# Performance work log

Measured on AMD Instinct MI355X. Metric: run time of the kernel, lower is better.

The kernel has to match this reference:

```python
import jax, jax.numpy as jnp
import numpy as np

B, S, T, E, H = 2, 2048, 2048, 1024, 16
D = E // H  # head_dim = 64


def setup_inputs() -> dict:
    key = jax.random.key(0)
    ks = jax.random.split(key, 11)
    scale = 1.0 / np.sqrt(E)
    return {
        "query": jax.random.normal(ks[0], (B, S, E), jnp.float32),
        "value": jax.random.normal(ks[1], (B, T, E), jnp.float32),
        "key": jax.random.normal(ks[2], (B, T, E), jnp.float32),
        "Wq": jax.random.normal(ks[3], (E, E), jnp.float32) * scale,
        "bq": jnp.zeros((E,), jnp.float32),
        "Wk": jax.random.normal(ks[4], (E, E), jnp.float32) * scale,
        "bk": jnp.zeros((E,), jnp.float32),
        "Wv": jax.random.normal(ks[5], (E, E), jnp.float32) * scale,
        "bv": jnp.zeros((E,), jnp.float32),
        "Wo": jax.random.normal(ks[6], (E, E), jnp.float32) * scale,
        "bo": jnp.zeros((E,), jnp.float32),
    }


def reference(query, value, key, Wq, bq, Wk, bk, Wv, bv, Wo, bo):
    b, s, e = query.shape
    t = value.shape[1]
    # linear projections (torch Linear: x @ W.T + b)
    q = query @ Wq.T + bq
    k = key @ Wk.T + bk
    v = value @ Wv.T + bv
    # split heads: [B, H, S, D]
    q = q.reshape(b, s, H, D).transpose(0, 2, 1, 3)
    k = k.reshape(b, t, H, D).transpose(0, 2, 1, 3)
    v = v.reshape(b, t, H, D).transpose(0, 2, 1, 3)
    # scaled dot-product attention; full [B,H,S,T] scores as in the original
    A = jnp.einsum("bhsd,bhtd->bhst", q, k) / jnp.sqrt(jnp.float32(D))
    A = jax.nn.softmax(A, axis=-1)
    # dropout p=0.0 -> identity
    out = jnp.einsum("bhst,bhtd->bhsd", A, v)
    out = out.transpose(0, 2, 1, 3).reshape(b, s, e)
    return out @ Wo.T + bo
```

## Files before the change

### kernel.cpp

```cpp
#include <hip/hip_runtime.h>
#include <math.h>

typedef __attribute__((ext_vector_type(8))) short short8;
typedef __attribute__((ext_vector_type(4))) float f32x4;
typedef unsigned short u16;

__device__ __forceinline__ u16 f2bf(float x) {
    unsigned int u = __float_as_uint(x);
    u += 0x7FFFu + ((u >> 16) & 1u);
    return (u16)(u >> 16);
}

__device__ __forceinline__ unsigned cvt_pk_bf16(float lo, float hi) {
    unsigned r;
    asm("v_cvt_pk_bf16_f32 %0, %1, %2" : "=v"(r) : "v"(lo), "v"(hi));
    return r;
}

__device__ __forceinline__ void load_lds16(const void* g, void* l) {
    __builtin_amdgcn_global_load_lds(
        (const __attribute__((address_space(1))) unsigned int*)g,
        (__attribute__((address_space(3))) unsigned int*)l,
        16, 0, 0);
}

struct CvtArgs {
    const float* src[7];
    u16* dst[7];
    int n8[7];
};

__global__ __launch_bounds__(256) void cvt_bf16(CvtArgs c) {
    const int z = blockIdx.z;
    const int i = blockIdx.x * 256 + threadIdx.x;
    if (i >= c.n8[z]) return;
    const float4* s = (const float4*)c.src[z];
    const float4 a = s[2 * i];
    const float4 b = s[2 * i + 1];
    union { short8 v; unsigned u[4]; } o;
    o.u[0] = cvt_pk_bf16(a.x, a.y);
    o.u[1] = cvt_pk_bf16(a.z, a.w);
    o.u[2] = cvt_pk_bf16(b.x, b.y);
    o.u[3] = cvt_pk_bf16(b.z, b.w);
    ((short8*)c.dst[z])[i] = o.v;
}

struct GemmArgs {
    const u16* A[3];
    const u16* W[3];
    const float* bias[3];
    void* C[3];
    float scale[3];
    int trans[3];
};

template <bool BF16OUT>
__global__ __launch_bounds__(256) void gemm_nt_mfma(GemmArgs ga, int M, int N, int K)
{
    __shared__ u16 As[128 * 32];
    __shared__ u16 Bs[128 * 32];
    const int z = blockIdx.z;
    const u16* __restrict__ A = ga.A[z];
    const u16* __restrict__ W = ga.W[z];
    const float* __restrict__ bias = ga.bias[z];
    const float scale = ga.scale[z];
    const int trans = ga.trans[z];

    const int tid = threadIdx.x;
    const int w = tid >> 6, l = tid & 63;
    const int l4 = l >> 4, lm = l & 15;
    const int wr = w >> 1, wc = w & 1;

    const int idx = blockIdx.x;
    const int xcd = idx & 7;
    const int sl  = idx >> 3;
    const int bmi = xcd * 4 + (sl & 3);
    const int bni = sl >> 2;
    const int bm = (trans ? bni : bmi) * 128;
    const int bn = (trans ? bmi : bni) * 128;

    const int srow = l >> 2;
    const int sseg = l & 3;

    f32x4 acc[4][4];
#pragma unroll
    for (int m = 0; m < 4; ++m)
#pragma unroll
        for (int n = 0; n < 4; ++n) acc[m][n] = (f32x4){0.f, 0.f, 0.f, 0.f};

    for (int k0 = 0; k0 < K; k0 += 32) {
        __syncthreads();
#pragma unroll
        for (int i = 0; i < 2; ++i) {
            const int blk = w * 2 + i;
            const int row = blk * 16 + srow;
            load_lds16(A + (size_t)(bm + row) * K + k0 + sseg * 8,
                       (char*)As + blk * 1024);
            load_lds16(W + (size_t)(bn + row) * K + k0 + sseg * 8,
                       (char*)Bs + blk * 1024);
        }
        __syncthreads();

        short8 af[4], bf[4];
#pragma unroll
        for (int m = 0; m < 4; ++m)
            af[m] = *(const short8*)&As[(wr * 64 + m * 16 + lm) * 32 + l4 * 8];
#pragma unroll
        for (int n = 0; n < 4; ++n)
            bf[n] = *(const short8*)&Bs[(wc * 64 + n * 16 + lm) * 32 + l4 * 8];
#pragma unroll
        for (int m = 0; m < 4; ++m)
#pragma unroll
            for (int n = 0; n < 4; ++n)
                acc[m][n] = __builtin_amdgcn_mfma_f32_16x16x32_bf16(af[m], bf[n], acc[m][n], 0, 0, 0);
    }

    if (!trans) {
        float bv[4];
#pragma unroll
        for (int n = 0; n < 4; ++n) bv[n] = bias[bn + wc * 64 + n * 16 + lm];
#pragma unroll
        for (int m = 0; m < 4; ++m) {
#pragma unroll
            for (int n = 0; n < 4; ++n) {
                const int col = bn + wc * 64 + n * 16 + lm;
#pragma unroll
                for (int r = 0; r < 4; ++r) {
                    const int row = bm + wr * 64 + m * 16 + l4 * 4 + r;
                    const float v = (acc[m][n][r] + bv[n]) * scale;
                    if (BF16OUT)
                        ((u16*)ga.C[z])[(size_t)row * N + col] = f2bf(v);
                    else
                        ((float*)ga.C[z])[(size_t)row * N + col] = v;
                }
            }
        }
    } else {
#pragma unroll
        for (int m = 0; m < 4; ++m) {
            const float4 bv4 = *(const float4*)(bias + bm + wr * 64 + m * 16 + l4 * 4);
            const float bvr[4] = {bv4.x, bv4.y, bv4.z, bv4.w};
#pragma unroll
            for (int n = 0; n < 4; ++n) {
                const int col = bn + wc * 64 + n * 16 + lm;
                const size_t cbase = (size_t)(col >> 11) * 2097152 + (size_t)(col & 2047);
#pragma unroll
                for (int r = 0; r < 4; ++r) {
                    const int row = bm + wr * 64 + m * 16 + l4 * 4 + r;
                    const float v = (acc[m][n][r] + bvr[r]) * scale;
                    ((u16*)ga.C[z])[cbase + (size_t)row * 2048] = f2bf(v);
                }
            }
        }
    }
}

__global__ __launch_bounds__(512, 4) void flash_attn_mfma8(
    const u16* __restrict__ Qb, const u16* __restrict__ Kb,
    const u16* __restrict__ Vt, u16* __restrict__ Ob)
{
    __shared__ u16 Ks[2][128 * 64];
    __shared__ u16 Vs[2][64 * 128];

    const int tid = threadIdx.x;
    const int w  = tid >> 6;
    const int l  = tid & 63;
    const int l4 = l >> 4;
    const int lm = l & 15;

    const int id = blockIdx.x;
    const int xcd = id & 7;
    const int s = id >> 3;
    const int qt = s & 15;
    const int g0 = (s >> 4) * 8 + xcd;
    const int h = g0 & 15;
    const int b = g0 >> 4;
    const int qb0 = qt << 7;

    const size_t bbase = (size_t)b * 2048 * 1024 + (size_t)h * 64;
    const size_t vbase = (size_t)b * 2097152 + (size_t)(h * 64) * 2048;

    short8 qf[2];
    {
        const u16* qrow = Qb + bbase + (size_t)(qb0 + w * 16 + lm) * 1024;
        qf[0] = *(const short8*)(qrow + l4 * 8);
        qf[1] = *(const short8*)(qrow + 32 + l4 * 8);
    }

    auto stageK = [&](int t0, int bufi) {
#pragma unroll
        for (int ii = 0; ii < 2; ++ii) {
            const int i = w * 2 + ii;
            const int key = i * 8 + (l >> 3);
            const int chunk = (l & 7) ^ ((l >> 3) & 7);
            load_lds16(Kb + bbase + (size_t)(t0 + key) * 1024 + chunk * 8,
                       (char*)&Ks[bufi][0] + i * 1024);
        }
    };
    auto stageV = [&](int t0, int bufi) {
#pragma unroll
        for (int ii = 0; ii < 2; ++ii) {
            const int i = w * 2 + ii;
            const int d = i * 4 + (l >> 4);
            const int chunk = (l & 15) ^ (d & 7);
            load_lds16(Vt + vbase + (size_t)d * 2048 + t0 + chunk * 8,
                       (char*)&Vs[bufi][0] + i * 1024);
        }
    };

    f32x4 oacc[4];
#pragma unroll
    for (int g = 0; g < 4; ++g) oacc[g] = (f32x4){0.f, 0.f, 0.f, 0.f};
    float m_run = -1e30f;
    float l_run = 0.f;

    stageK(0, 0);
    stageV(0, 0);

    for (int t = 0; t < 16; ++t) {
        const int buf = t & 1;
        if (t < 15) {
            stageK((t + 1) * 128, buf ^ 1);
            stageV((t + 1) * 128, buf ^ 1);
            asm volatile("s_waitcnt vmcnt(4)" ::: "memory");
        } else {
            asm volatile("s_waitcnt vmcnt(0)" ::: "memory");
        }
        __builtin_amdgcn_s_barrier();

        f32x4 sacc[8];
#pragma unroll
        for (int g = 0; g < 8; ++g) sacc[g] = (f32x4){0.f, 0.f, 0.f, 0.f};
        __builtin_amdgcn_s_setprio(1);
#pragma unroll
        for (int g = 0; g < 8; ++g) {
#pragma unroll
            for (int c = 0; c < 2; ++c) {
                const short8 kf = *(const short8*)
                    &Ks[buf][(16 * g + lm) * 64 + (((4 * c + l4) ^ (lm & 7)) << 3)];
                sacc[g] = __builtin_amdgcn_mfma_f32_16x16x32_bf16(kf, qf[c], sacc[g], 0, 0, 0);
            }
        }
        __builtin_amdgcn_s_setprio(0);

        float amax[8];
#pragma unroll
        for (int g = 0; g < 8; ++g)
            amax[g] = fmaxf(fmaxf(sacc[g][0], sacc[g][1]), fmaxf(sacc[g][2], sacc[g][3]));
        float mt = fmaxf(fmaxf(fmaxf(amax[0], amax[1]), fmaxf(amax[2], amax[3])),
                         fmaxf(fmaxf(amax[4], amax[5]), fmaxf(amax[6], amax[7])));
        mt = fmaxf(mt, __shfl_xor(mt, 16));
        mt = fmaxf(mt, __shfl_xor(mt, 32));

        const bool resc = !__all(mt <= m_run + 8.0f);
        if (resc) {
            const float mn = fmaxf(m_run, mt);
            const float alpha = __builtin_amdgcn_exp2f(m_run - mn);
            m_run = mn;
            l_run *= alpha;
#pragma unroll
            for (int r = 0; r < 4; ++r) {
                const float a = __shfl(alpha, l4 * 4 + r);
#pragma unroll
                for (int g = 0; g < 4; ++g) oacc[g][r] *= a;
            }
        }

        float lsum = 0.f;
        const float mr = m_run;
        unsigned up[8], vp[8];
#pragma unroll
        for (int g = 0; g < 8; ++g) {
            const float p0 = __builtin_amdgcn_exp2f(sacc[g][0] - mr);
            const float p1 = __builtin_amdgcn_exp2f(sacc[g][1] - mr);
            const float p2 = __builtin_amdgcn_exp2f(sacc[g][2] - mr);
            const float p3 = __builtin_amdgcn_exp2f(sacc[g][3] - mr);
            lsum += (p0 + p1) + (p2 + p3);
            up[g] = cvt_pk_bf16(p0, p1);
            vp[g] = cvt_pk_bf16(p2, p3);
        }
        lsum += __shfl_xor(lsum, 16);
        lsum += __shfl_xor(lsum, 32);
        l_run += lsum;

#pragma unroll
        for (int kb = 0; kb < 4; ++kb) {
            unsigned w0 = up[2 * kb], w2 = up[2 * kb + 1];
            unsigned w1 = vp[2 * kb], w3 = vp[2 * kb + 1];
            asm("v_permlane32_swap_b32 %0, %1" : "+v"(w0), "+v"(w2));
            asm("v_permlane16_swap_b32 %0, %1" : "+v"(w0), "+v"(w2));
            asm("v_permlane32_swap_b32 %0, %1" : "+v"(w1), "+v"(w3));
            asm("v_permlane16_swap_b32 %0, %1" : "+v"(w1), "+v"(w3));
            union { unsigned u[4]; short8 v8; } pa;
            pa.u[0] = w0; pa.u[1] = w1; pa.u[2] = w2; pa.u[3] = w3;
            __builtin_amdgcn_s_setprio(1);
#pragma unroll
            for (int g = 0; g < 4; ++g) {
                const int d = 16 * g + lm;
                const short8 vf = *(const short8*)
                    &Vs[buf][d * 128 + (((kb * 4 + l4) ^ (d & 7)) << 3)];
                oacc[g] = __builtin_amdgcn_mfma_f32_16x16x32_bf16(pa.v8, vf, oacc[g], 0, 0, 0);
            }
            __builtin_amdgcn_s_setprio(0);
        }

        __builtin_amdgcn_s_barrier();
    }

#pragma unroll
    for (int r = 0; r < 4; ++r) {
        const float linv = 1.f / __shfl(l_run, l4 * 4 + r);
        const size_t orow = bbase + (size_t)(qb0 + w * 16 + l4 * 4 + r) * 1024;
#pragma unroll
        for (int g = 0; g < 4; ++g)
            Ob[orow + g * 16 + lm] = f2bf(oacc[g][r] * linv);
    }
}

extern "C" void kernel_launch(void* const* d_in, const int* in_sizes, int n_in,
                              void* d_out, int out_size, void* d_ws, size_t ws_size,
                              hipStream_t stream)
{
    const float* query = (const float*)d_in[0];
    const float* value = (const float*)d_in[1];
    const float* key   = (const float*)d_in[2];
    const float* Wq = (const float*)d_in[3];
    const float* bq = (const float*)d_in[4];
    const float* Wk = (const float*)d_in[5];
    const float* bk = (const float*)d_in[6];
    const float* Wv = (const float*)d_in[7];
    const float* bv = (const float*)d_in[8];
    const float* Wo = (const float*)d_in[9];
    const float* bo = (const float*)d_in[10];
    float* out = (float*)d_out;

    const int M = 2 * 2048;
    const int E = 1024;
    const size_t act = (size_t)M * E;
    const size_t wel = (size_t)E * E;

    u16* qc  = (u16*)d_ws;
    u16* kc  = qc + act;
    u16* vc  = kc + act;
    u16* wqb = vc + act;
    u16* wkb = wqb + wel;
    u16* wvb = wkb + wel;
    u16* wob = wvb + wel;
    u16* Qb  = wob + wel;
    u16* Kb  = Qb + act;
    u16* Vtb = Kb + act;
    u16* Ab  = Vtb + act;

    CvtArgs ca;
    ca.src[0] = query; ca.dst[0] = qc;  ca.n8[0] = (int)(act / 8);
    ca.src[1] = key;   ca.dst[1] = kc;  ca.n8[1] = (int)(act / 8);
    ca.src[2] = value; ca.dst[2] = vc;  ca.n8[2] = (int)(act / 8);
    ca.src[3] = Wq;    ca.dst[3] = wqb; ca.n8[3] = (int)(wel / 8);
    ca.src[4] = Wk;    ca.dst[4] = wkb; ca.n8[4] = (int)(wel / 8);
    ca.src[5] = Wv;    ca.dst[5] = wvb; ca.n8[5] = (int)(wel / 8);
    ca.src[6] = Wo;    ca.dst[6] = wob; ca.n8[6] = (int)(wel / 8);
    dim3 cgrid((unsigned)((act / 8 + 255) / 256), 1, 7);
    hipLaunchKernelGGL(cvt_bf16, cgrid, dim3(256), 0, stream, ca);

    const float SCALE_Q = 0.125f * 1.4426950408889634f;

    GemmArgs gq;
    gq.A[0] = qc;  gq.W[0] = wqb; gq.bias[0] = bq; gq.C[0] = Qb;  gq.scale[0] = SCALE_Q; gq.trans[0] = 0;
    gq.A[1] = kc;  gq.W[1] = wkb; gq.bias[1] = bk; gq.C[1] = Kb;  gq.scale[1] = 1.0f;    gq.trans[1] = 0;
    gq.A[2] = wvb; gq.W[2] = vc;  gq.bias[2] = bv; gq.C[2] = Vtb; gq.scale[2] = 1.0f;    gq.trans[2] = 1;
    hipLaunchKernelGGL((gemm_nt_mfma<true>), dim3(256, 1, 3), dim3(256), 0, stream, gq, M, E, E);

    hipLaunchKernelGGL(flash_attn_mfma8, dim3(512), dim3(512), 0, stream, Qb, Kb, Vtb, Ab);

    GemmArgs go;
    go.A[0] = Ab; go.W[0] = wob; go.bias[0] = bo; go.C[0] = out; go.scale[0] = 1.0f; go.trans[0] = 0;
    go.A[1] = Ab; go.W[1] = wob; go.bias[1] = bo; go.C[1] = out; go.scale[1] = 1.0f; go.trans[1] = 0;
    go.A[2] = Ab; go.W[2] = wob; go.bias[2] = bo; go.C[2] = out; go.scale[2] = 1.0f; go.trans[2] = 0;
    hipLaunchKernelGGL((gemm_nt_mfma<false>), dim3(256, 1, 1), dim3(256), 0, stream, go, M, E, E);
}
```

Measured before the change: 147.0 us.

## Switch flash attention to 32x32x16 MFMA with 4 waves of 32 query rows

Rewrites the attention kernel to use 32x32x16 bf16 MFMA instead of 16x16x32. Each wave now owns 32 query rows, and the block drops from 8 waves to 4. Fragment layouts, softmax reductions, the P permutation (only a permlane32 swap), rescaling and output indexing are all reworked to match. The aim is to cut the number of LDS fragment reads and MFMA instructions per FLOP and to reduce cross-lane shuffles. In exchange each wave holds more accumulator registers, and occupancy may drop to fewer waves per CU.

```diff
diff --git a/kernel.cpp b/kernel.cpp
--- a/kernel.cpp
+++ b/kernel.cpp
@@ -3,6 +3,7 @@
 
 typedef __attribute__((ext_vector_type(8))) short short8;
 typedef __attribute__((ext_vector_type(4))) float f32x4;
+typedef __attribute__((ext_vector_type(16))) float f32x16;
 typedef unsigned short u16;
 
 __device__ __forceinline__ u16 f2bf(float x) {
@@ -155,7 +156,7 @@
     }
 }
 
-__global__ __launch_bounds__(512, 4) void flash_attn_mfma8(
+__global__ __launch_bounds__(256, 2) void flash_attn_mfma9(
     const u16* __restrict__ Qb, const u16* __restrict__ Kb,
     const u16* __restrict__ Vt, u16* __restrict__ Ob)
 {
@@ -165,8 +166,8 @@
     const int tid = threadIdx.x;
     const int w  = tid >> 6;
     const int l  = tid & 63;
-    const int l4 = l >> 4;
-    const int lm = l & 15;
+    const int hi = l >> 5;
+    const int lq = l & 31;
 
     const int id = blockIdx.x;
     const int xcd = id & 7;
@@ -180,17 +181,18 @@
     const size_t bbase = (size_t)b * 2048 * 1024 + (size_t)h * 64;
     const size_t vbase = (size_t)b * 2097152 + (size_t)(h * 64) * 2048;
 
-    short8 qf[2];
+    short8 qf[4];
     {
-        const u16* qrow = Qb + bbase + (size_t)(qb0 + w * 16 + lm) * 1024;
-        qf[0] = *(const short8*)(qrow + l4 * 8);
-        qf[1] = *(const short8*)(qrow + 32 + l4 * 8);
+        const u16* qrow = Qb + bbase + (size_t)(qb0 + w * 32 + lq) * 1024;
+#pragma unroll
+        for (int t = 0; t < 4; ++t)
+            qf[t] = *(const short8*)(qrow + t * 16 + hi * 8);
     }
 
     auto stageK = [&](int t0, int bufi) {
 #pragma unroll
-        for (int ii = 0; ii < 2; ++ii) {
-            const int i = w * 2 + ii;
+        for (int ii = 0; ii < 4; ++ii) {
+            const int i = w * 4 + ii;
             const int key = i * 8 + (l >> 3);
             const int chunk = (l & 7) ^ ((l >> 3) & 7);
             load_lds16(Kb + bbase + (size_t)(t0 + key) * 1024 + chunk * 8,
@@ -199,8 +201,8 @@
     };
     auto stageV = [&](int t0, int bufi) {
 #pragma unroll
-        for (int ii = 0; ii < 2; ++ii) {
-            const int i = w * 2 + ii;
+        for (int ii = 0; ii < 4; ++ii) {
+            const int i = w * 4 + ii;
             const int d = i * 4 + (l >> 4);
             const int chunk = (l & 15) ^ (d & 7);
             load_lds16(Vt + vbase + (size_t)d * 2048 + t0 + chunk * 8,
@@ -208,9 +210,7 @@
         }
     };
 
-    f32x4 oacc[4];
-#pragma unroll
-    for (int g = 0; g < 4; ++g) oacc[g] = (f32x4){0.f, 0.f, 0.f, 0.f};
+    f32x16 oacc[2] = {{}, {}};
     float m_run = -1e30f;
     float l_run = 0.f;
 
@@ -222,34 +222,31 @@
         if (t < 15) {
             stageK((t + 1) * 128, buf ^ 1);
             stageV((t + 1) * 128, buf ^ 1);
-            asm volatile("s_waitcnt vmcnt(4)" ::: "memory");
+            asm volatile("s_waitcnt vmcnt(8)" ::: "memory");
         } else {
             asm volatile("s_waitcnt vmcnt(0)" ::: "memory");
         }
         __builtin_amdgcn_s_barrier();
 
-        f32x4 sacc[8];
-#pragma unroll
-        for (int g = 0; g < 8; ++g) sacc[g] = (f32x4){0.f, 0.f, 0.f, 0.f};
+        f32x16 sacc[4] = {{}, {}, {}, {}};
         __builtin_amdgcn_s_setprio(1);
 #pragma unroll
-        for (int g = 0; g < 8; ++g) {
-#pragma unroll
-            for (int c = 0; c < 2; ++c) {
+        for (int kb = 0; kb < 4; ++kb) {
+#pragma unroll
+            for (int tt = 0; tt < 4; ++tt) {
                 const short8 kf = *(const short8*)
-                    &Ks[buf][(16 * g + lm) * 64 + (((4 * c + l4) ^ (lm & 7)) << 3)];
-                sacc[g] = __builtin_amdgcn_mfma_f32_16x16x32_bf16(kf, qf[c], sacc[g], 0, 0, 0);
+                    &Ks[buf][(32 * kb + lq) * 64 + (((2 * tt + hi) ^ (l & 7)) << 3)];
+                sacc[kb] = __builtin_amdgcn_mfma_f32_32x32x16_bf16(kf, qf[tt], sacc[kb], 0, 0, 0);
             }
         }
         __builtin_amdgcn_s_setprio(0);
 
-        float amax[8];
-#pragma unroll
-        for (int g = 0; g < 8; ++g)
-            amax[g] = fmaxf(fmaxf(sacc[g][0], sacc[g][1]), fmaxf(sacc[g][2], sacc[g][3]));
-        float mt = fmaxf(fmaxf(fmaxf(amax[0], amax[1]), fmaxf(amax[2], amax[3])),
-                         fmaxf(fmaxf(amax[4], amax[5]), fmaxf(amax[6], amax[7])));
-        mt = fmaxf(mt, __shfl_xor(mt, 16));
+        float mt = sacc[0][0];
+#pragma unroll
+        for (int kb = 0; kb < 4; ++kb)
+#pragma unroll
+            for (int r = 0; r < 16; ++r)
+                mt = fmaxf(mt, sacc[kb][r]);
         mt = fmaxf(mt, __shfl_xor(mt, 32));
 
         const bool resc = !__all(mt <= m_run + 8.0f);
@@ -259,61 +256,65 @@
             m_run = mn;
             l_run *= alpha;
 #pragma unroll
-            for (int r = 0; r < 4; ++r) {
-                const float a = __shfl(alpha, l4 * 4 + r);
-#pragma unroll
-                for (int g = 0; g < 4; ++g) oacc[g][r] *= a;
+            for (int r = 0; r < 16; ++r) {
+                const float a = __shfl(alpha, (r & 3) + 8 * (r >> 2) + 4 * hi);
+                oacc[0][r] *= a;
+                oacc[1][r] *= a;
             }
         }
 
         float lsum = 0.f;
         const float mr = m_run;
-        unsigned up[8], vp[8];
-#pragma unroll
-        for (int g = 0; g < 8; ++g) {
-            const float p0 = __builtin_amdgcn_exp2f(sacc[g][0] - mr);
-            const float p1 = __builtin_amdgcn_exp2f(sacc[g][1] - mr);
-            const float p2 = __builtin_amdgcn_exp2f(sacc[g][2] - mr);
-            const float p3 = __builtin_amdgcn_exp2f(sacc[g][3] - mr);
-            lsum += (p0 + p1) + (p2 + p3);
-            up[g] = cvt_pk_bf16(p0, p1);
-            vp[g] = cvt_pk_bf16(p2, p3);
-        }
-        lsum += __shfl_xor(lsum, 16);
+        unsigned wlo[4][4], whi[4][4];
+#pragma unroll
+        for (int kb = 0; kb < 4; ++kb) {
+#pragma unroll
+            for (int qd = 0; qd < 4; ++qd) {
+                const float p0 = __builtin_amdgcn_exp2f(sacc[kb][4 * qd + 0] - mr);
+                const float p1 = __builtin_amdgcn_exp2f(sacc[kb][4 * qd + 1] - mr);
+                const float p2 = __builtin_amdgcn_exp2f(sacc[kb][4 * qd + 2] - mr);
+                const float p3 = __builtin_amdgcn_exp2f(sacc[kb][4 * qd + 3] - mr);
+                lsum += (p0 + p1) + (p2 + p3);
+                wlo[kb][qd] = cvt_pk_bf16(p0, p1);
+                whi[kb][qd] = cvt_pk_bf16(p2, p3);
+            }
+        }
         lsum += __shfl_xor(lsum, 32);
         l_run += lsum;
 
 #pragma unroll
         for (int kb = 0; kb < 4; ++kb) {
-            unsigned w0 = up[2 * kb], w2 = up[2 * kb + 1];
-            unsigned w1 = vp[2 * kb], w3 = vp[2 * kb + 1];
-            asm("v_permlane32_swap_b32 %0, %1" : "+v"(w0), "+v"(w2));
-            asm("v_permlane16_swap_b32 %0, %1" : "+v"(w0), "+v"(w2));
-            asm("v_permlane32_swap_b32 %0, %1" : "+v"(w1), "+v"(w3));
-            asm("v_permlane16_swap_b32 %0, %1" : "+v"(w1), "+v"(w3));
-            union { unsigned u[4]; short8 v8; } pa;
-            pa.u[0] = w0; pa.u[1] = w1; pa.u[2] = w2; pa.u[3] = w3;
-            __builtin_amdgcn_s_setprio(1);
-#pragma unroll
-            for (int g = 0; g < 4; ++g) {
-                const int d = 16 * g + lm;
-                const short8 vf = *(const short8*)
-                    &Vs[buf][d * 128 + (((kb * 4 + l4) ^ (d & 7)) << 3)];
-                oacc[g] = __builtin_amdgcn_mfma_f32_16x16x32_bf16(pa.v8, vf, oacc[g], 0, 0, 0);
-            }
-            __builtin_amdgcn_s_setprio(0);
+#pragma unroll
+            for (int u = 0; u < 2; ++u) {
+                unsigned X  = wlo[kb][2 * u], Y  = wlo[kb][2 * u + 1];
+                unsigned X2 = whi[kb][2 * u], Y2 = whi[kb][2 * u + 1];
+                asm("v_permlane32_swap_b32 %0, %1" : "+v"(X),  "+v"(Y));
+                asm("v_permlane32_swap_b32 %0, %1" : "+v"(X2), "+v"(Y2));
+                union { unsigned u4[4]; short8 v8; } pa;
+                pa.u4[0] = X; pa.u4[1] = X2; pa.u4[2] = Y; pa.u4[3] = Y2;
+                const int sstep = 2 * kb + u;
+                __builtin_amdgcn_s_setprio(1);
+#pragma unroll
+                for (int g = 0; g < 2; ++g) {
+                    const int d = 32 * g + lq;
+                    const short8 vf = *(const short8*)
+                        &Vs[buf][d * 128 + (((2 * sstep + hi) ^ (d & 7)) << 3)];
+                    oacc[g] = __builtin_amdgcn_mfma_f32_32x32x16_bf16(pa.v8, vf, oacc[g], 0, 0, 0);
+                }
+                __builtin_amdgcn_s_setprio(0);
+            }
         }
 
         __builtin_amdgcn_s_barrier();
     }
 
 #pragma unroll
-    for (int r = 0; r < 4; ++r) {
-        const float linv = 1.f / __shfl(l_run, l4 * 4 + r);
-        const size_t orow = bbase + (size_t)(qb0 + w * 16 + l4 * 4 + r) * 1024;
-#pragma unroll
-        for (int g = 0; g < 4; ++g)
-            Ob[orow + g * 16 + lm] = f2bf(oacc[g][r] * linv);
+    for (int r = 0; r < 16; ++r) {
+        const int row = (r & 3) + 8 * (r >> 2) + 4 * hi;
+        const float linv = 1.f / __shfl(l_run, row);
+        const size_t orow = bbase + (size_t)(qb0 + w * 32 + row) * 1024;
+        Ob[orow + lq]      = f2bf(oacc[0][r] * linv);
+        Ob[orow + 32 + lq] = f2bf(oacc[1][r] * linv);
     }
 }
 
@@ -370,7 +371,7 @@
     gq.A[2] = wvb; gq.W[2] = vc;  gq.bias[2] = bv; gq.C[2] = Vtb; gq.scale[2] = 1.0f;    gq.trans[2] = 1;
     hipLaunchKernelGGL((gemm_nt_mfma<true>), dim3(256, 1, 3), dim3(256), 0, stream, gq, M, E, E);
 
-    hipLaunchKernelGGL(flash_attn_mfma8, dim3(512), dim3(512), 0, stream, Qb, Kb, Vtb, Ab);
+    hipLaunchKernelGGL(flash_attn_mfma9, dim3(512), dim3(256), 0, stream, Qb, Kb, Vtb, Ab);
 
     GemmArgs go;
     go.A[0] = Ab; go.W[0] = wob; go.bias[0] = bo; go.C[0] = out; go.scale[0] = 1.0f; go.trans[0] = 0;
```

Measured after the change: 145.4 us. No clear change (-1.0%).
